# Performance work log

Measured on AMD Instinct MI355X. Metric: run time of the kernel, lower is better.

Reference implementation:

```python
import jax, jax.numpy as jnp
import numpy as np

CD_WEIGHT = 100.0


def setup_inputs() -> dict:
    key = jax.random.key(0)
    k1, k2 = jax.random.split(key)
    array1 = jax.random.normal(k1, (4, 4096, 3), dtype=jnp.float32)
    array2 = jax.random.normal(k2, (4, 4096, 3), dtype=jnp.float32)
    return {"array1": array1, "array2": array2}


def _chamfer(a1, a2):
    # a1: [B, N, D], a2: [B, M, D]
    # squared pairwise distances d2[b, n, m] = ||a1[b,n] - a2[b,m]||^2
    # computed as ||a||^2 + ||b||^2 - 2 a.b to avoid materializing [B,N,M,D]
    sq1 = jnp.sum(a1 * a1, axis=-1)                      # [B, N]
    sq2 = jnp.sum(a2 * a2, axis=-1)                      # [B, M]
    cross = jnp.einsum("bnd,bmd->bnm", a1, a2)           # [B, N, M]
    d2 = sq1[:, :, None] + sq2[:, None, :] - 2.0 * cross  # [B, N, M]
    # av_dist1: for each array2 point, min over array1 points, then mean
    av_dist1 = jnp.mean(jnp.min(d2, axis=1), axis=-1)    # [B]
    # av_dist2: for each array1 point, min over array2 points, then mean
    av_dist2 = jnp.mean(jnp.min(d2, axis=2), axis=-1)    # [B]
    return CD_WEIGHT * jnp.mean(0.5 * (av_dist1 + av_dist2))


def reference(array1, array2):
    return _chamfer(array1, array2)
```

## Files before the change

### kernel.cpp

```cpp
#include <hip/hip_runtime.h>
#include <math.h>


typedef __attribute__((ext_vector_type(8))) short bf16x8;
typedef __attribute__((ext_vector_type(4))) float f32x4;

#define NPTS    4096
#define NBATCH  4
#define MCHUNK  1024
#define NSUPER  64
#define ONE_BF  ((short)0x3F80)
#define SCALE   (50.0f / (float)(NBATCH * NPTS))

__device__ __forceinline__ unsigned short bf_rne(float v) {
    unsigned int u = __float_as_uint(v);
    u += 0x7FFFu + ((u >> 16) & 1u);
    return (unsigned short)(u >> 16);
}
__device__ __forceinline__ float bf_f(unsigned short s) {
    return __uint_as_float(((unsigned int)s) << 16);
}
__device__ __forceinline__ void split2(float v, short& h, short& l) {
    unsigned short hh = bf_rne(v);
    h = (short)hh;
    l = (short)bf_rne(v - bf_f(hh));
}

__global__ __launch_bounds__(256, 4) void chamfer_mfma(
    const float* __restrict__ a1, const float* __restrict__ a2,
    unsigned int* __restrict__ grow, unsigned int* __restrict__ gcol)
{
    __shared__ bf16x8 Bp0[MCHUNK + 1];
    __shared__ bf16x8 Bp1[MCHUNK];
    __shared__ bf16x8 Ap0[NSUPER + 1];
    __shared__ bf16x8 Ap1[NSUPER];

    const int bid = blockIdx.x;
    const int mc  = bid & 3;
    const int ns  = (bid >> 2) & 63;
    const int b   = bid >> 8;
    const int tid = threadIdx.x;

    const float* rb = a2 + ((size_t)b * NPTS + (size_t)mc * MCHUNK) * 3;
    #pragma unroll
    for (int i = 0; i < MCHUNK / 256; ++i) {
        const int m = tid + i * 256;
        float x = rb[3 * m + 0], y = rb[3 * m + 1], z = rb[3 * m + 2];
        float r2 = fmaf(x, x, fmaf(y, y, z * z));
        short xh, xl, yh, yl, zh, zl, rh, rl;
        split2(x, xh, xl); split2(y, yh, yl); split2(z, zh, zl);
        split2(r2, rh, rl);
        bf16x8 p0 = {xh, yh, zh, xh, yh, zh, xl, yl};
        bf16x8 p1 = {zl, ONE_BF, ONE_BF, rh, rl, 0, 0, 0};
        Bp0[m] = p0; Bp1[m] = p1;
    }
    if (tid < NSUPER) {
        const float* qa = a1 + ((size_t)b * NPTS + (size_t)ns * NSUPER) * 3;
        float x = qa[3 * tid + 0], y = qa[3 * tid + 1], z = qa[3 * tid + 2];
        float q2 = fmaf(x, x, fmaf(y, y, z * z));
        short axh, axl, ayh, ayl, azh, azl, qh, ql;
        split2(-2.0f * x, axh, axl);
        split2(-2.0f * y, ayh, ayl);
        split2(-2.0f * z, azh, azl);
        split2(q2, qh, ql);
        bf16x8 p0 = {axh, ayh, azh, axl, ayl, azl, axh, ayh};
        bf16x8 p1 = {azh, qh, ql, ONE_BF, 0, 0, 0, 0};
        Ap0[tid] = p0; Ap1[tid] = p1;
    }
    __syncthreads();

    const int w    = tid >> 6;
    const int lane = tid & 63;
    const int quad = lane >> 4;
    const int c    = lane & 15;

    const bf16x8 zf = {0, 0, 0, 0, 0, 0, 0, 0};
    const f32x4  zc = {0.f, 0.f, 0.f, 0.f};

    bf16x8 af0 = zf, af1 = zf, af2 = zf, af3 = zf;
    if (quad == 0) { af0 = Ap0[c]; af1 = Ap0[16 + c]; af2 = Ap0[32 + c]; af3 = Ap0[48 + c]; }
    else if (quad == 1) { af0 = Ap1[c]; af1 = Ap1[16 + c]; af2 = Ap1[32 + c]; af3 = Ap1[48 + c]; }

    float rowacc[16];
    #pragma unroll
    for (int r = 0; r < 16; ++r) rowacc[r] = INFINITY;

    unsigned int* gcolb = gcol + b * NPTS + mc * MCHUNK;

    #pragma unroll 4
    for (int mt = 0; mt < 16; ++mt) {
        const int mb = w * 256 + mt * 16;
        bf16x8 bfr = zf;
        if (quad == 0)      bfr = Bp0[mb + c];
        else if (quad == 1) bfr = Bp1[mb + c];

        float colT = INFINITY;
        f32x4 d;
        d = __builtin_amdgcn_mfma_f32_16x16x32_bf16(af0, bfr, zc, 0, 0, 0);
        rowacc[0] = fminf(rowacc[0], d[0]);  rowacc[1] = fminf(rowacc[1], d[1]);
        rowacc[2] = fminf(rowacc[2], d[2]);  rowacc[3] = fminf(rowacc[3], d[3]);
        colT = fminf(colT, fminf(fminf(d[0], d[1]), fminf(d[2], d[3])));
        d = __builtin_amdgcn_mfma_f32_16x16x32_bf16(af1, bfr, zc, 0, 0, 0);
        rowacc[4] = fminf(rowacc[4], d[0]);  rowacc[5] = fminf(rowacc[5], d[1]);
        rowacc[6] = fminf(rowacc[6], d[2]);  rowacc[7] = fminf(rowacc[7], d[3]);
        colT = fminf(colT, fminf(fminf(d[0], d[1]), fminf(d[2], d[3])));
        d = __builtin_amdgcn_mfma_f32_16x16x32_bf16(af2, bfr, zc, 0, 0, 0);
        rowacc[8] = fminf(rowacc[8], d[0]);  rowacc[9] = fminf(rowacc[9], d[1]);
        rowacc[10] = fminf(rowacc[10], d[2]); rowacc[11] = fminf(rowacc[11], d[3]);
        colT = fminf(colT, fminf(fminf(d[0], d[1]), fminf(d[2], d[3])));
        d = __builtin_amdgcn_mfma_f32_16x16x32_bf16(af3, bfr, zc, 0, 0, 0);
        rowacc[12] = fminf(rowacc[12], d[0]); rowacc[13] = fminf(rowacc[13], d[1]);
        rowacc[14] = fminf(rowacc[14], d[2]); rowacc[15] = fminf(rowacc[15], d[3]);
        colT = fminf(colT, fminf(fminf(d[0], d[1]), fminf(d[2], d[3])));

        colT = fminf(colT, __shfl_xor(colT, 16));
        colT = fminf(colT, __shfl_xor(colT, 32));
        if (quad == 0)
            atomicMin(&gcolb[mb + c], __float_as_uint(fmaxf(colT, 0.f)));
    }

    #pragma unroll
    for (int st = 1; st <= 8; st <<= 1) {
        #pragma unroll
        for (int r = 0; r < 16; ++r)
            rowacc[r] = fminf(rowacc[r], __shfl_xor(rowacc[r], st));
    }
    if (c == 0) {
        #pragma unroll
        for (int r = 0; r < 16; ++r) {
            const int row = ns * NSUPER + (r >> 2) * 16 + quad * 4 + (r & 3);
            atomicMin(&grow[b * NPTS + row],
                      __float_as_uint(fmaxf(rowacc[r], 0.f)));
        }
    }
}

__global__ __launch_bounds__(1024) void chamfer_final(
    const unsigned int* __restrict__ gmin, float* __restrict__ out)
{
    float s = 0.0f;
    for (int i = threadIdx.x; i < 2 * NBATCH * NPTS; i += 1024)
        s += __uint_as_float(gmin[i]);
    for (int off = 32; off > 0; off >>= 1) s += __shfl_down(s, off);
    __shared__ float wsum[16];
    if ((threadIdx.x & 63) == 0) wsum[threadIdx.x >> 6] = s;
    __syncthreads();
    if (threadIdx.x < 64) {
        float v = (threadIdx.x < 16) ? wsum[threadIdx.x] : 0.0f;
        for (int off = 8; off > 0; off >>= 1) v += __shfl_down(v, off);
        if (threadIdx.x == 0) out[0] = v * SCALE;
    }
}

extern "C" void kernel_launch(void* const* d_in, const int* in_sizes, int n_in,
                              void* d_out, int out_size, void* d_ws, size_t ws_size,
                              hipStream_t stream) {
    const float* a1 = (const float*)d_in[0];
    const float* a2 = (const float*)d_in[1];
    float* out = (float*)d_out;
    unsigned int* grow = (unsigned int*)d_ws;
    unsigned int* gcol = grow + NBATCH * NPTS;

    chamfer_mfma<<<NBATCH * 64 * 4, 256, 0, stream>>>(a1, a2, grow, gcol);
    chamfer_final<<<1, 1024, 0, stream>>>(grow, out);
}
```

Measured before the change: 74.83 us.

## Compute both chamfer directions as row-min passes, dropping global atomics

The kernel no longer computes row and column minima from one distance tile with atomicMin into global buffers. It launches separate blocks for each direction: each block owns 64 query points and loops over all 4096 reference points in 1024-point LDS chunks. Each block reduces its minima in LDS and writes them with plain stores. This removes global atomics, the cross-lane column reductions and the dependence on zero-initialized workspace, but doubles the MFMA distance work and the bf16 splitting of reference points.

```diff
diff --git a/kernel.cpp b/kernel.cpp
--- a/kernel.cpp
+++ b/kernel.cpp
@@ -7,8 +7,9 @@
 
 #define NPTS    4096
 #define NBATCH  4
-#define MCHUNK  1024
-#define NSUPER  64
+#define QG      64
+#define CHUNK   1024
+#define NCHUNK  (NPTS / CHUNK)
 #define ONE_BF  ((short)0x3F80)
 #define SCALE   (50.0f / (float)(NBATCH * NPTS))
 
@@ -28,35 +29,33 @@
 
 __global__ __launch_bounds__(256, 4) void chamfer_mfma(
     const float* __restrict__ a1, const float* __restrict__ a2,
-    unsigned int* __restrict__ grow, unsigned int* __restrict__ gcol)
+    float* __restrict__ rmins)
 {
-    __shared__ bf16x8 Bp0[MCHUNK + 1];
-    __shared__ bf16x8 Bp1[MCHUNK];
-    __shared__ bf16x8 Ap0[NSUPER + 1];
-    __shared__ bf16x8 Ap1[NSUPER];
+    __shared__ bf16x8 Bp0[CHUNK];
+    __shared__ bf16x8 Bp1[CHUNK];
+    __shared__ bf16x8 Ap0[QG];
+    __shared__ bf16x8 Ap1[QG];
+    __shared__ float  pm2[4][QG];
 
     const int bid = blockIdx.x;
-    const int mc  = bid & 3;
-    const int ns  = (bid >> 2) & 63;
-    const int b   = bid >> 8;
-    const int tid = threadIdx.x;
+    const int rg  = bid & 63;
+    const int b   = (bid >> 6) & 3;
+    const int dir = bid >> 8;
+    const float* q = (dir == 0) ? a1 : a2;
+    const float* r = (dir == 0) ? a2 : a1;
+    const float* qbase = q + ((size_t)b * NPTS + (size_t)rg * QG) * 3;
+    const float* rbase = r + (size_t)b * NPTS * 3;
 
-    const float* rb = a2 + ((size_t)b * NPTS + (size_t)mc * MCHUNK) * 3;
-    #pragma unroll
-    for (int i = 0; i < MCHUNK / 256; ++i) {
-        const int m = tid + i * 256;
-        float x = rb[3 * m + 0], y = rb[3 * m + 1], z = rb[3 * m + 2];
-        float r2 = fmaf(x, x, fmaf(y, y, z * z));
-        short xh, xl, yh, yl, zh, zl, rh, rl;
-        split2(x, xh, xl); split2(y, yh, yl); split2(z, zh, zl);
-        split2(r2, rh, rl);
-        bf16x8 p0 = {xh, yh, zh, xh, yh, zh, xl, yl};
-        bf16x8 p1 = {zl, ONE_BF, ONE_BF, rh, rl, 0, 0, 0};
-        Bp0[m] = p0; Bp1[m] = p1;
-    }
-    if (tid < NSUPER) {
-        const float* qa = a1 + ((size_t)b * NPTS + (size_t)ns * NSUPER) * 3;
-        float x = qa[3 * tid + 0], y = qa[3 * tid + 1], z = qa[3 * tid + 2];
+    const int tid  = threadIdx.x;
+    const int w    = tid >> 6;
+    const int lane = tid & 63;
+    const int quad = lane >> 4;
+    const int c    = lane & 15;
+
+    if (tid < QG) {
+        float x = qbase[3 * tid + 0];
+        float y = qbase[3 * tid + 1];
+        float z = qbase[3 * tid + 2];
         float q2 = fmaf(x, x, fmaf(y, y, z * z));
         short axh, axl, ayh, ayl, azh, azl, qh, ql;
         split2(-2.0f * x, axh, axl);
@@ -67,80 +66,93 @@
         bf16x8 p1 = {azh, qh, ql, ONE_BF, 0, 0, 0, 0};
         Ap0[tid] = p0; Ap1[tid] = p1;
     }
-    __syncthreads();
-
-    const int w    = tid >> 6;
-    const int lane = tid & 63;
-    const int quad = lane >> 4;
-    const int c    = lane & 15;
 
     const bf16x8 zf = {0, 0, 0, 0, 0, 0, 0, 0};
     const f32x4  zc = {0.f, 0.f, 0.f, 0.f};
 
     bf16x8 af0 = zf, af1 = zf, af2 = zf, af3 = zf;
-    if (quad == 0) { af0 = Ap0[c]; af1 = Ap0[16 + c]; af2 = Ap0[32 + c]; af3 = Ap0[48 + c]; }
-    else if (quad == 1) { af0 = Ap1[c]; af1 = Ap1[16 + c]; af2 = Ap1[32 + c]; af3 = Ap1[48 + c]; }
-
     float rowacc[16];
     #pragma unroll
-    for (int r = 0; r < 16; ++r) rowacc[r] = INFINITY;
+    for (int i = 0; i < 16; ++i) rowacc[i] = INFINITY;
 
-    unsigned int* gcolb = gcol + b * NPTS + mc * MCHUNK;
+    for (int ch = 0; ch < NCHUNK; ++ch) {
+        if (ch) __syncthreads();
+        #pragma unroll
+        for (int i = 0; i < CHUNK / 256; ++i) {
+            const int m = tid + i * 256;
+            const int g = ch * CHUNK + m;
+            float x = rbase[3 * g + 0];
+            float y = rbase[3 * g + 1];
+            float z = rbase[3 * g + 2];
+            float r2 = fmaf(x, x, fmaf(y, y, z * z));
+            short xh, xl, yh, yl, zh, zl, rh, rl;
+            split2(x, xh, xl); split2(y, yh, yl); split2(z, zh, zl);
+            split2(r2, rh, rl);
+            bf16x8 p0 = {xh, yh, zh, xh, yh, zh, xl, yl};
+            bf16x8 p1 = {zl, ONE_BF, ONE_BF, rh, rl, 0, 0, 0};
+            Bp0[m] = p0; Bp1[m] = p1;
+        }
+        __syncthreads();
 
-    #pragma unroll 4
-    for (int mt = 0; mt < 16; ++mt) {
-        const int mb = w * 256 + mt * 16;
-        bf16x8 bfr = zf;
-        if (quad == 0)      bfr = Bp0[mb + c];
-        else if (quad == 1) bfr = Bp1[mb + c];
+        if (ch == 0) {
+            if (quad == 0) {
+                af0 = Ap0[c]; af1 = Ap0[16 + c];
+                af2 = Ap0[32 + c]; af3 = Ap0[48 + c];
+            } else if (quad == 1) {
+                af0 = Ap1[c]; af1 = Ap1[16 + c];
+                af2 = Ap1[32 + c]; af3 = Ap1[48 + c];
+            }
+        }
 
-        float colT = INFINITY;
-        f32x4 d;
-        d = __builtin_amdgcn_mfma_f32_16x16x32_bf16(af0, bfr, zc, 0, 0, 0);
-        rowacc[0] = fminf(rowacc[0], d[0]);  rowacc[1] = fminf(rowacc[1], d[1]);
-        rowacc[2] = fminf(rowacc[2], d[2]);  rowacc[3] = fminf(rowacc[3], d[3]);
-        colT = fminf(colT, fminf(fminf(d[0], d[1]), fminf(d[2], d[3])));
-        d = __builtin_amdgcn_mfma_f32_16x16x32_bf16(af1, bfr, zc, 0, 0, 0);
-        rowacc[4] = fminf(rowacc[4], d[0]);  rowacc[5] = fminf(rowacc[5], d[1]);
-        rowacc[6] = fminf(rowacc[6], d[2]);  rowacc[7] = fminf(rowacc[7], d[3]);
-        colT = fminf(colT, fminf(fminf(d[0], d[1]), fminf(d[2], d[3])));
-        d = __builtin_amdgcn_mfma_f32_16x16x32_bf16(af2, bfr, zc, 0, 0, 0);
-        rowacc[8] = fminf(rowacc[8], d[0]);  rowacc[9] = fminf(rowacc[9], d[1]);
-        rowacc[10] = fminf(rowacc[10], d[2]); rowacc[11] = fminf(rowacc[11], d[3]);
-        colT = fminf(colT, fminf(fminf(d[0], d[1]), fminf(d[2], d[3])));
-        d = __builtin_amdgcn_mfma_f32_16x16x32_bf16(af3, bfr, zc, 0, 0, 0);
-        rowacc[12] = fminf(rowacc[12], d[0]); rowacc[13] = fminf(rowacc[13], d[1]);
-        rowacc[14] = fminf(rowacc[14], d[2]); rowacc[15] = fminf(rowacc[15], d[3]);
-        colT = fminf(colT, fminf(fminf(d[0], d[1]), fminf(d[2], d[3])));
+        #pragma unroll 4
+        for (int ct = 0; ct < 16; ++ct) {
+            const int mb = (ct * 4 + w) * 16;
+            bf16x8 bfr = zf;
+            if (quad == 0)      bfr = Bp0[mb + c];
+            else if (quad == 1) bfr = Bp1[mb + c];
 
-        colT = fminf(colT, __shfl_xor(colT, 16));
-        colT = fminf(colT, __shfl_xor(colT, 32));
-        if (quad == 0)
-            atomicMin(&gcolb[mb + c], __float_as_uint(fmaxf(colT, 0.f)));
+            f32x4 d;
+            d = __builtin_amdgcn_mfma_f32_16x16x32_bf16(af0, bfr, zc, 0, 0, 0);
+            rowacc[0] = fminf(rowacc[0], d[0]);  rowacc[1] = fminf(rowacc[1], d[1]);
+            rowacc[2] = fminf(rowacc[2], d[2]);  rowacc[3] = fminf(rowacc[3], d[3]);
+            d = __builtin_amdgcn_mfma_f32_16x16x32_bf16(af1, bfr, zc, 0, 0, 0);
+            rowacc[4] = fminf(rowacc[4], d[0]);  rowacc[5] = fminf(rowacc[5], d[1]);
+            rowacc[6] = fminf(rowacc[6], d[2]);  rowacc[7] = fminf(rowacc[7], d[3]);
+            d = __builtin_amdgcn_mfma_f32_16x16x32_bf16(af2, bfr, zc, 0, 0, 0);
+            rowacc[8] = fminf(rowacc[8], d[0]);  rowacc[9] = fminf(rowacc[9], d[1]);
+            rowacc[10] = fminf(rowacc[10], d[2]); rowacc[11] = fminf(rowacc[11], d[3]);
+            d = __builtin_amdgcn_mfma_f32_16x16x32_bf16(af3, bfr, zc, 0, 0, 0);
+            rowacc[12] = fminf(rowacc[12], d[0]); rowacc[13] = fminf(rowacc[13], d[1]);
+            rowacc[14] = fminf(rowacc[14], d[2]); rowacc[15] = fminf(rowacc[15], d[3]);
+        }
     }
 
     #pragma unroll
     for (int st = 1; st <= 8; st <<= 1) {
         #pragma unroll
-        for (int r = 0; r < 16; ++r)
-            rowacc[r] = fminf(rowacc[r], __shfl_xor(rowacc[r], st));
+        for (int i = 0; i < 16; ++i)
+            rowacc[i] = fminf(rowacc[i], __shfl_xor(rowacc[i], st));
     }
     if (c == 0) {
         #pragma unroll
-        for (int r = 0; r < 16; ++r) {
-            const int row = ns * NSUPER + (r >> 2) * 16 + quad * 4 + (r & 3);
-            atomicMin(&grow[b * NPTS + row],
-                      __float_as_uint(fmaxf(rowacc[r], 0.f)));
-        }
+        for (int i = 0; i < 16; ++i)
+            pm2[w][(i >> 2) * 16 + quad * 4 + (i & 3)] = rowacc[i];
+    }
+    __syncthreads();
+
+    if (tid < QG) {
+        float m = fminf(fminf(pm2[0][tid], pm2[1][tid]),
+                        fminf(pm2[2][tid], pm2[3][tid]));
+        rmins[(size_t)bid * QG + tid] = fmaxf(m, 0.0f);
     }
 }
 
 __global__ __launch_bounds__(1024) void chamfer_final(
-    const unsigned int* __restrict__ gmin, float* __restrict__ out)
+    const float* __restrict__ rmins, float* __restrict__ out)
 {
     float s = 0.0f;
     for (int i = threadIdx.x; i < 2 * NBATCH * NPTS; i += 1024)
-        s += __uint_as_float(gmin[i]);
+        s += rmins[i];
     for (int off = 32; off > 0; off >>= 1) s += __shfl_down(s, off);
     __shared__ float wsum[16];
     if ((threadIdx.x & 63) == 0) wsum[threadIdx.x >> 6] = s;
@@ -157,10 +169,9 @@
                               hipStream_t stream) {
     const float* a1 = (const float*)d_in[0];
     const float* a2 = (const float*)d_in[1];
-    float* out = (float*)d_out;
-    unsigned int* grow = (unsigned int*)d_ws;
-    unsigned int* gcol = grow + NBATCH * NPTS;
+    float* out   = (float*)d_out;
+    float* rmins = (float*)d_ws;
 
-    chamfer_mfma<<<NBATCH * 64 * 4, 256, 0, stream>>>(a1, a2, grow, gcol);
-    chamfer_final<<<1, 1024, 0, stream>>>(grow, out);
+    chamfer_mfma<<<2 * NBATCH * (NPTS / QG), 256, 0, stream>>>(a1, a2, rmins);
+    chamfer_final<<<1, 1024, 0, stream>>>(rmins, out);
 }
```

Result: slower. 80.45 us (+7.5%).
